# Kernel tuning notes

Hardware: AMD Instinct MI355X
Metric: run time of the kernel (lower is better)

Reference implementation:

```python
import jax, jax.numpy as jnp
import numpy as np

N, E, H, G, L = 100000, 200000, 32, 100, 4
NODE_IN, EDGE_IN, NGRAPH = 6, 4, 50
EPS = 1e-5

def setup_inputs() -> dict:
    key = jax.random.key(0)
    ks = jax.random.split(key, 32)
    s = 0.05
    inp = {
        "x": jax.random.normal(ks[0], (N, NODE_IN), jnp.float32),
        "edge_index": jax.random.randint(ks[1], (2, E), 0, N, jnp.int64),
        "edge_attr": jax.random.normal(ks[2], (E, EDGE_IN), jnp.float32),
        "batch": jnp.sort(jax.random.randint(ks[3], (N,), 0, NGRAPH, jnp.int64)),
        # node embedding: Linear + ReLU + BatchNorm1d
        "w_embed": jax.random.normal(ks[4], (NODE_IN, H), jnp.float32) * s,
        "b_embed": jnp.zeros((H,), jnp.float32),
        "bn_gamma": jnp.ones((H,), jnp.float32),
        "bn_beta": jnp.zeros((H,), jnp.float32),
        # NNConv layers (stacked over L): edge MLP Linear(EDGE_IN,2H)->ReLU->Linear(2H,H*H), root weight, bias
        "conv_w1": jax.random.normal(ks[5], (L, EDGE_IN, 2 * H), jnp.float32) * s,
        "conv_b1": jnp.zeros((L, 2 * H), jnp.float32),
        "conv_w2": jax.random.normal(ks[6], (L, 2 * H, H * H), jnp.float32) * s,
        "conv_b2": jnp.zeros((L, H * H), jnp.float32),
        "conv_root": jax.random.normal(ks[7], (L, H, H), jnp.float32) * s,
        "conv_bias": jnp.zeros((L, H), jnp.float32),
        # heads
        "wk_w1": jax.random.normal(ks[8], (H, H), jnp.float32) * s,
        "wk_b1": jnp.zeros((H,), jnp.float32),
        "wk_w2": jax.random.normal(ks[9], (H, 1), jnp.float32) * s,
        "wk_b2": jnp.zeros((1,), jnp.float32),
        "uj_w1": jax.random.normal(ks[10], (H, H), jnp.float32) * s,
        "uj_b1": jnp.zeros((H,), jnp.float32),
        "uj_w2": jax.random.normal(ks[11], (H, G), jnp.float32) * s,
        "uj_b2": jnp.zeros((G,), jnp.float32),
        "zk_w1": jax.random.normal(ks[12], (H, H), jnp.float32) * s,
        "zk_b1": jnp.zeros((H,), jnp.float32),
        "zk_w2": jax.random.normal(ks[13], (H, G), jnp.float32) * s,
        "zk_b2": jnp.zeros((G,), jnp.float32),
    }
    return inp

def _mlp2(h, w1, b1, w2, b2):
    return jax.nn.relu(h @ w1 + b1) @ w2 + b2

def _forward(x, edge_index, edge_attr, batch,
             w_embed, b_embed, bn_gamma, bn_beta,
             conv_w1, conv_b1, conv_w2, conv_b2, conv_root, conv_bias,
             wk_w1, wk_b1, wk_w2, wk_b2,
             uj_w1, uj_b1, uj_w2, uj_b2,
             zk_w1, zk_b1, zk_w2, zk_b2):
    src, dst = edge_index[0], edge_index[1]
    # node embed: Linear -> ReLU -> BatchNorm1d (training-mode batch stats)
    h = jax.nn.relu(x @ w_embed + b_embed)
    mu = h.mean(axis=0)
    var = ((h - mu) ** 2).mean(axis=0)  # biased, as torch BN uses for normalization
    h = (h - mu) * jax.lax.rsqrt(var + EPS) * bn_gamma + bn_beta
    # in-degree for mean aggregation
    deg = jax.ops.segment_sum(jnp.ones((E,), h.dtype), dst, num_segments=N)
    inv_deg = (1.0 / jnp.maximum(deg, 1.0))[:, None]
    for l in range(L):
        # per-edge weight matrix from edge MLP: [E, H, H]
        W = _mlp2(edge_attr, conv_w1[l], conv_b1[l], conv_w2[l], conv_b2[l]).reshape(E, H, H)
        msg = jnp.einsum('ei,eio->eo', h[src], W)  # gather + per-edge matmul
        agg = jax.ops.segment_sum(msg, dst, num_segments=N) * inv_deg  # scatter-mean
        h = jax.nn.relu(agg + h @ conv_root[l] + conv_bias[l])
    # global mean pool over graphs
    cnt = jax.ops.segment_sum(jnp.ones((N,), h.dtype), batch, num_segments=NGRAPH)
    hg = jax.ops.segment_sum(h, batch, num_segments=NGRAPH) / jnp.maximum(cnt, 1.0)[:, None]
    wk = _mlp2(hg, wk_w1, wk_b1, wk_w2, wk_b2).squeeze(-1)
    uj = _mlp2(hg, uj_w1, uj_b1, uj_w2, uj_b2)
    zk = _mlp2(hg, zk_w1, zk_b1, zk_w2, zk_b2)
    return wk, uj, zk

def reference(x, edge_index, edge_attr, batch,
              w_embed, b_embed, bn_gamma, bn_beta,
              conv_w1, conv_b1, conv_w2, conv_b2, conv_root, conv_bias,
              wk_w1, wk_b1, wk_w2, wk_b2,
              uj_w1, uj_b1, uj_w2, uj_b2,
              zk_w1, zk_b1, zk_w2, zk_b2):
    return _forward(x, edge_index, edge_attr, batch,
                    w_embed, b_embed, bn_gamma, bn_beta,
                    conv_w1, conv_b1, conv_w2, conv_b2, conv_root, conv_bias,
                    wk_w1, wk_b1, wk_w2, wk_b2,
                    uj_w1, uj_b1, uj_w2, uj_b2,
                    zk_w1, zk_b1, zk_w2, zk_b2)
```

## Files before the change

### kernel.cpp

```cpp
#include <hip/hip_runtime.h>

#define NN 100000
#define NE 200000
#define HH 32
#define NL 4
#define NGR 50
#define GOUT 100
#define NODE_IN 6
#define NEB 782

typedef __attribute__((ext_vector_type(8))) short bf16x8;
typedef __attribute__((ext_vector_type(4))) float f32x4;

__device__ __forceinline__ unsigned short bf16_rne(float x) {
    unsigned int b = __float_as_uint(x);
    b += 0x7FFFu + ((b >> 16) & 1u);
    return (unsigned short)(b >> 16);
}
__device__ __forceinline__ float bf16_f(unsigned short h) {
    return __uint_as_float(((unsigned int)h) << 16);
}

__global__ __launch_bounds__(256) void split_w2(const float* __restrict__ w2,
                                                unsigned short* __restrict__ w2h,
                                                unsigned short* __restrict__ w2l)
{
    int id = blockIdx.x * 256 + threadIdx.x;
    if (id >= NL * 64 * 1024) return;
    int l = id >> 16, rem = id & 65535;
    int k = rem >> 10, n = rem & 1023;
    float v = w2[id];
    unsigned short hi = bf16_rne(v);
    float lov = v - bf16_f(hi);
    unsigned short lo = bf16_rne(lov);
    int out = l * 65536 + n * 64 + k;
    w2h[out] = hi;
    w2l[out] = lo;
}

__global__ __launch_bounds__(256) void embed_kernel(
    const float* __restrict__ x, const float* __restrict__ w,
    const float* __restrict__ b, float* __restrict__ h0)
{
    int nid = blockIdx.x * 256 + threadIdx.x;
    if (nid >= NN) return;
    float xv[NODE_IN];
    #pragma unroll
    for (int d = 0; d < NODE_IN; ++d) xv[d] = x[nid * NODE_IN + d];
    float4* op = (float4*)(h0 + (size_t)nid * HH);
    #pragma unroll
    for (int q = 0; q < 8; ++q) {
        float4 r;
        float* rp = (float*)&r;
        #pragma unroll
        for (int u = 0; u < 4; ++u) {
            int j = q * 4 + u;
            float a = b[j];
            #pragma unroll
            for (int d = 0; d < NODE_IN; ++d) a = fmaf(xv[d], w[d * HH + j], a);
            rp[u] = fmaxf(a, 0.f);
        }
        op[q] = r;
    }
}

__global__ __launch_bounds__(256) void stats_kernel(const float* __restrict__ h0,
                                                    float* __restrict__ stats)
{
    __shared__ float ls[64];
    int tid = threadIdx.x;
    if (tid < 64) ls[tid] = 0.f;
    __syncthreads();
    float s[4] = {0.f, 0.f, 0.f, 0.f};
    float q[4] = {0.f, 0.f, 0.f, 0.f};
    const float4* h4 = (const float4*)h0;
    const int total = NN * HH / 4;
    for (int idx = blockIdx.x * 256 + tid; idx < total; idx += 128 * 256) {
        float4 v = h4[idx];
        s[0] += v.x; q[0] += v.x * v.x;
        s[1] += v.y; q[1] += v.y * v.y;
        s[2] += v.z; q[2] += v.z * v.z;
        s[3] += v.w; q[3] += v.w * v.w;
    }
    int c0 = (tid * 4) & 31;
    #pragma unroll
    for (int u = 0; u < 4; ++u) {
        atomicAdd(&ls[c0 + u], s[u]);
        atomicAdd(&ls[32 + c0 + u], q[u]);
    }
    __syncthreads();
    if (tid < 64) unsafeAtomicAdd(&stats[tid], ls[tid]);
}

__global__ __launch_bounds__(256) void deg_kernel(const int* __restrict__ ei,
                                                  float* __restrict__ deg)
{
    int e = blockIdx.x * 256 + threadIdx.x;
    if (e >= NE) return;
    unsafeAtomicAdd(&deg[ei[NE + e]], 1.0f);
}

__global__ void bn_finalize(const float* __restrict__ stats,
                            const float* __restrict__ gamma,
                            const float* __restrict__ beta,
                            float* __restrict__ bnp)
{
    int j = threadIdx.x;
    if (j >= HH) return;
    const float invn = 1.0f / (float)NN;
    float mu  = stats[j] * invn;
    float var = stats[32 + j] * invn - mu * mu;
    float rs  = 1.0f / sqrtf(var + 1e-5f);
    float sc  = rs * gamma[j];
    bnp[j]      = sc;
    bnp[32 + j] = beta[j] - mu * sc;
}

__global__ __launch_bounds__(256) void bn_apply(float* __restrict__ h,
                                                const float* __restrict__ bnp)
{
    int idx = blockIdx.x * 256 + threadIdx.x;
    if (idx >= NN * HH / 4) return;
    float4 v = ((float4*)h)[idx];
    int j = (idx * 4) & 31;
    v.x = fmaf(v.x, bnp[j + 0], bnp[32 + j + 0]);
    v.y = fmaf(v.y, bnp[j + 1], bnp[32 + j + 1]);
    v.z = fmaf(v.z, bnp[j + 2], bnp[32 + j + 2]);
    v.w = fmaf(v.w, bnp[j + 3], bnp[32 + j + 3]);
    ((float4*)h)[idx] = v;
}

__global__ __launch_bounds__(256) void edge_mfma(
    const float* __restrict__ h, const int* __restrict__ ei,
    const float* __restrict__ ea,
    const float* __restrict__ w1, const float* __restrict__ b1,
    const unsigned short* __restrict__ w2h, const unsigned short* __restrict__ w2l,
    const float* __restrict__ b2, float* __restrict__ agg)
{
    __shared__ float hT[32 * 256];
    __shared__ float b2l[1024];
    __shared__ int   dstl[256];
    __shared__ unsigned short Bh[2][4096];
    __shared__ unsigned short Bl[2][4096];

    const int tid  = threadIdx.x;
    const int w    = tid >> 6;
    const int lane = tid & 63;
    const int l15  = lane & 15;
    const int lg   = lane >> 4;
    const int eb   = blockIdx.x * 256;

    const unsigned int* gh = (const unsigned int*)w2h;
    const unsigned int* gl = (const unsigned int*)w2l;
    const int wavebase = tid & ~63;

    auto stage = [&](int c2, int buf) {
        #pragma unroll
        for (int q = 0; q < 2; ++q) {
            int g = q * 256 + tid;
            int n = g >> 3, j = g & 7;
            int gi = ((c2 * 64 + n) << 3) + (j ^ (n & 7));
            int lb = (q * 256 + wavebase) * 8;
            __builtin_amdgcn_global_load_lds(
                (const __attribute__((address_space(1))) unsigned int*)(gh + (size_t)gi * 4),
                (__attribute__((address_space(3))) unsigned int*)(&Bh[buf][0] + lb), 16, 0, 0);
            __builtin_amdgcn_global_load_lds(
                (const __attribute__((address_space(1))) unsigned int*)(gl + (size_t)gi * 4),
                (__attribute__((address_space(3))) unsigned int*)(&Bl[buf][0] + lb), 16, 0, 0);
        }
    };

    stage(0, 0);

    {
        int e = eb + tid;
        int s = 0, d = 0;
        if (e < NE) { s = ei[e]; d = ei[NE + e]; }
        dstl[tid] = d;
        const float4* hp = (const float4*)(h + (size_t)s * HH);
        #pragma unroll
        for (int q = 0; q < 8; ++q) {
            float4 v = hp[q];
            hT[(q * 4 + 0) * 256 + tid] = v.x;
            hT[(q * 4 + 1) * 256 + tid] = v.y;
            hT[(q * 4 + 2) * 256 + tid] = v.z;
            hT[(q * 4 + 3) * 256 + tid] = v.w;
        }
        ((float4*)b2l)[tid] = ((const float4*)b2)[tid];
    }

    bf16x8 thi[4][2], tlo[4][2];
    #pragma unroll
    for (int et = 0; et < 4; ++et) {
        int e = eb + w * 64 + et * 16 + l15;
        bool ev = (e < NE);
        float4 eav = make_float4(0.f, 0.f, 0.f, 0.f);
        if (ev) eav = *(const float4*)(ea + (size_t)e * 4);
        #pragma unroll
        for (int ks = 0; ks < 2; ++ks) {
            int k0 = ks * 32 + lg * 8;
            #pragma unroll
            for (int j = 0; j < 8; ++j) {
                float t = b1[k0 + j];
                t = fmaf(eav.x, w1[0 * 64 + k0 + j], t);
                t = fmaf(eav.y, w1[1 * 64 + k0 + j], t);
                t = fmaf(eav.z, w1[2 * 64 + k0 + j], t);
                t = fmaf(eav.w, w1[3 * 64 + k0 + j], t);
                t = ev ? fmaxf(t, 0.f) : 0.f;
                unsigned short hi = bf16_rne(t);
                float lov = t - bf16_f(hi);
                unsigned short lo = bf16_rne(lov);
                thi[et][ks][j] = (short)hi;
                tlo[et][ks][j] = (short)lo;
            }
        }
    }

    float acc0[4][4], acc1[4][4];
    #pragma unroll
    for (int et = 0; et < 4; ++et)
        #pragma unroll
        for (int r = 0; r < 4; ++r) { acc0[et][r] = 0.f; acc1[et][r] = 0.f; }

    for (int c2 = 0; c2 < 16; ++c2) {
        const int buf = c2 & 1;
        __syncthreads();
        if (c2 < 15) stage(c2 + 1, buf ^ 1);

        #pragma unroll
        for (int ntp = 0; ntp < 2; ++ntp) {
            const int i = c2 * 2 + ntp;
            float4 h4[4];
            #pragma unroll
            for (int et = 0; et < 4; ++et)
                h4[et] = *(const float4*)&hT[i * 256 + wavebase + et * 16 + lg * 4];
            #pragma unroll
            for (int half = 0; half < 2; ++half) {
                int nt = ntp * 2 + half;
                int nl = nt * 16 + l15;
                int swz = (nl & 7) << 4;
                const char* bhrow = (const char*)&Bh[buf][0] + nl * 128;
                const char* blrow = (const char*)&Bl[buf][0] + nl * 128;
                bf16x8 Bh0 = *(const bf16x8*)(bhrow + (( 0 + lg * 16) ^ swz));
                bf16x8 Bl0 = *(const bf16x8*)(blrow + (( 0 + lg * 16) ^ swz));
                bf16x8 Bh1 = *(const bf16x8*)(bhrow + ((64 + lg * 16) ^ swz));
                bf16x8 Bl1 = *(const bf16x8*)(blrow + ((64 + lg * 16) ^ swz));
                float b2v = b2l[c2 * 64 + nt * 16 + l15];
                #pragma unroll
                for (int et = 0; et < 4; ++et) {
                    f32x4 G = {0.f, 0.f, 0.f, 0.f};
                    G = __builtin_amdgcn_mfma_f32_16x16x32_bf16(thi[et][0], Bh0, G, 0, 0, 0);
                    G = __builtin_amdgcn_mfma_f32_16x16x32_bf16(tlo[et][0], Bh0, G, 0, 0, 0);
                    G = __builtin_amdgcn_mfma_f32_16x16x32_bf16(thi[et][0], Bl0, G, 0, 0, 0);
                    G = __builtin_amdgcn_mfma_f32_16x16x32_bf16(thi[et][1], Bh1, G, 0, 0, 0);
                    G = __builtin_amdgcn_mfma_f32_16x16x32_bf16(tlo[et][1], Bh1, G, 0, 0, 0);
                    G = __builtin_amdgcn_mfma_f32_16x16x32_bf16(thi[et][1], Bl1, G, 0, 0, 0);
                    if (half == 0) {
                        acc0[et][0] = fmaf(h4[et].x, G[0] + b2v, acc0[et][0]);
                        acc0[et][1] = fmaf(h4[et].y, G[1] + b2v, acc0[et][1]);
                        acc0[et][2] = fmaf(h4[et].z, G[2] + b2v, acc0[et][2]);
                        acc0[et][3] = fmaf(h4[et].w, G[3] + b2v, acc0[et][3]);
                    } else {
                        acc1[et][0] = fmaf(h4[et].x, G[0] + b2v, acc1[et][0]);
                        acc1[et][1] = fmaf(h4[et].y, G[1] + b2v, acc1[et][1]);
                        acc1[et][2] = fmaf(h4[et].z, G[2] + b2v, acc1[et][2]);
                        acc1[et][3] = fmaf(h4[et].w, G[3] + b2v, acc1[et][3]);
                    }
                }
            }
        }
    }

    #pragma unroll
    for (int et = 0; et < 4; ++et) {
        int eloc = wavebase + et * 16 + lg * 4;
        int4 d4 = *(const int4*)&dstl[eloc];
        #pragma unroll
        for (int r = 0; r < 4; ++r) {
            int eg = eb + eloc + r;
            if (eg < NE) {
                int dd = (r == 0) ? d4.x : (r == 1) ? d4.y : (r == 2) ? d4.z : d4.w;
                unsafeAtomicAdd(agg + (size_t)dd * HH + l15,      acc0[et][r]);
                unsafeAtomicAdd(agg + (size_t)dd * HH + 16 + l15, acc1[et][r]);
            }
        }
    }
}

__global__ __launch_bounds__(256) void node_kernel(
    const float* __restrict__ h, const float* __restrict__ agg,
    const float* __restrict__ deg, const float* __restrict__ root,
    const float* __restrict__ bias, float* __restrict__ hout)
{
    int nid = blockIdx.x * 256 + threadIdx.x;
    if (nid >= NN) return;
    float hv[HH];
    {
        const float4* hp = (const float4*)(h + nid * HH);
        #pragma unroll
        for (int q = 0; q < 8; ++q) {
            float4 v = hp[q];
            hv[4*q+0] = v.x; hv[4*q+1] = v.y; hv[4*q+2] = v.z; hv[4*q+3] = v.w;
        }
    }
    float inv = 1.0f / fmaxf(deg[nid], 1.0f);
    float acc[HH];
    #pragma unroll
    for (int o = 0; o < HH; ++o) acc[o] = bias[o];
    #pragma unroll
    for (int i = 0; i < HH; ++i) {
        float hi = hv[i];
        #pragma unroll
        for (int o = 0; o < HH; ++o) acc[o] = fmaf(hi, root[i * HH + o], acc[o]);
    }
    const float4* av = (const float4*)(agg + nid * HH);
    #pragma unroll
    for (int q = 0; q < 8; ++q) {
        float4 a = av[q];
        float4 r;
        r.x = fmaxf(fmaf(a.x, inv, acc[4*q+0]), 0.f);
        r.y = fmaxf(fmaf(a.y, inv, acc[4*q+1]), 0.f);
        r.z = fmaxf(fmaf(a.z, inv, acc[4*q+2]), 0.f);
        r.w = fmaxf(fmaf(a.w, inv, acc[4*q+3]), 0.f);
        ((float4*)(hout + nid * HH))[q] = r;
    }
}

__global__ __launch_bounds__(256) void pool_kernel(
    const float* __restrict__ h, const int* __restrict__ batch,
    float* __restrict__ pool, float* __restrict__ cnt)
{
    __shared__ float lp[NGR * HH];
    __shared__ float lc[NGR];
    int tid = threadIdx.x;
    for (int i = tid; i < NGR * HH; i += 256) lp[i] = 0.f;
    for (int i = tid; i < NGR; i += 256) lc[i] = 0.f;
    __syncthreads();
    int nid = blockIdx.x * 256 + tid;
    if (nid < NN) {
        int g = batch[nid];
        atomicAdd(&lc[g], 1.0f);
        #pragma unroll
        for (int j = 0; j < HH; ++j) atomicAdd(&lp[g * HH + j], h[nid * HH + j]);
    }
    __syncthreads();
    for (int i = tid; i < NGR * HH; i += 256)
        if (lp[i] != 0.f) unsafeAtomicAdd(&pool[i], lp[i]);
    for (int i = tid; i < NGR; i += 256)
        if (lc[i] != 0.f) unsafeAtomicAdd(&cnt[i], lc[i]);
}

__global__ __launch_bounds__(256) void heads_kernel(
    const float* __restrict__ pool, const float* __restrict__ cnt,
    const float* __restrict__ wkw1, const float* __restrict__ wkb1,
    const float* __restrict__ wkw2, const float* __restrict__ wkb2,
    const float* __restrict__ ujw1, const float* __restrict__ ujb1,
    const float* __restrict__ ujw2, const float* __restrict__ ujb2,
    const float* __restrict__ zkw1, const float* __restrict__ zkb1,
    const float* __restrict__ zkw2, const float* __restrict__ zkb2,
    float* __restrict__ out)
{
    __shared__ float hg[NGR * HH];
    __shared__ float hid[NGR * HH];
    int tid = threadIdx.x;
    int head = blockIdx.x;
    const float *w1, *b1, *w2, *b2;
    if (head == 0)      { w1 = wkw1; b1 = wkb1; w2 = wkw2; b2 = wkb2; }
    else if (head == 1) { w1 = ujw1; b1 = ujb1; w2 = ujw2; b2 = ujb2; }
    else                { w1 = zkw1; b1 = zkb1; w2 = zkw2; b2 = zkb2; }
    for (int i = tid; i < NGR * HH; i += 256) {
        int g = i >> 5;
        hg[i] = pool[i] / fmaxf(cnt[g], 1.0f);
    }
    __syncthreads();
    for (int i = tid; i < NGR * HH; i += 256) {
        int g = i >> 5, c = i & 31;
        float a = b1[c];
        for (int j = 0; j < HH; ++j) a = fmaf(hg[g * HH + j], w1[j * HH + c], a);
        hid[i] = fmaxf(a, 0.f);
    }
    __syncthreads();
    if (head == 0) {
        if (tid < NGR) {
            float a = b2[0];
            for (int c = 0; c < HH; ++c) a = fmaf(hid[tid * HH + c], w2[c], a);
            out[tid] = a;
        }
    } else {
        float* ob = out + NGR + (head - 1) * NGR * GOUT;
        for (int i = tid; i < NGR * GOUT; i += 256) {
            int g = i / GOUT, u = i % GOUT;
            float a = b2[u];
            for (int c = 0; c < HH; ++c) a = fmaf(hid[g * HH + c], w2[c * GOUT + u], a);
            ob[i] = a;
        }
    }
}

extern "C" void kernel_launch(void* const* d_in, const int* in_sizes, int n_in,
                              void* d_out, int out_size, void* d_ws, size_t ws_size,
                              hipStream_t stream)
{
    const float* x     = (const float*)d_in[0];
    const int*   ei    = (const int*)d_in[1];
    const float* ea    = (const float*)d_in[2];
    const int*   batch = (const int*)d_in[3];
    const float* w_emb = (const float*)d_in[4];
    const float* b_emb = (const float*)d_in[5];
    const float* gamma = (const float*)d_in[6];
    const float* beta  = (const float*)d_in[7];
    const float* cw1   = (const float*)d_in[8];
    const float* cb1   = (const float*)d_in[9];
    const float* cw2   = (const float*)d_in[10];
    const float* cb2   = (const float*)d_in[11];
    const float* croot = (const float*)d_in[12];
    const float* cbias = (const float*)d_in[13];
    float* out = (float*)d_out;

    unsigned short* w2h = (unsigned short*)d_ws;
    unsigned short* w2l = w2h + (size_t)NL * 65536;
    float* h0    = (float*)(w2l + (size_t)NL * 65536);
    float* h1    = h0 + (size_t)NN * HH;
    float* agg   = h1 + (size_t)NN * HH;
    float* deg   = agg + (size_t)NN * HH;
    float* stats = deg + NN;
    float* pool  = stats + 64;
    float* cnt   = pool + NGR * HH;
    float* bnp   = cnt + NGR;

    hipMemsetAsync(deg, 0, (size_t)(NN + 64 + NGR * HH + NGR) * sizeof(float), stream);

    split_w2<<<(NL * 65536) / 256, 256, 0, stream>>>(cw2, w2h, w2l);
    embed_kernel<<<(NN + 255) / 256, 256, 0, stream>>>(x, w_emb, b_emb, h0);
    stats_kernel<<<128, 256, 0, stream>>>(h0, stats);
    deg_kernel<<<(NE + 255) / 256, 256, 0, stream>>>(ei, deg);
    bn_finalize<<<1, 32, 0, stream>>>(stats, gamma, beta, bnp);
    bn_apply<<<(NN * HH / 4 + 255) / 256, 256, 0, stream>>>(h0, bnp);

    float* hc = h0;
    float* hn = h1;
    for (int l = 0; l < NL; ++l) {
        hipMemsetAsync(agg, 0, (size_t)NN * HH * sizeof(float), stream);
        edge_mfma<<<NEB, 256, 0, stream>>>(
            hc, ei, ea,
            cw1 + (size_t)l * 4 * 64, cb1 + (size_t)l * 64,
            w2h + (size_t)l * 65536, w2l + (size_t)l * 65536,
            cb2 + (size_t)l * 1024, agg);
        node_kernel<<<(NN + 255) / 256, 256, 0, stream>>>(
            hc, agg, deg, croot + (size_t)l * HH * HH, cbias + (size_t)l * HH, hn);
        float* t = hc; hc = hn; hn = t;
    }

    pool_kernel<<<(NN + 255) / 256, 256, 0, stream>>>(hc, batch, pool, cnt);
    heads_kernel<<<3, 256, 0, stream>>>(pool, cnt,
        (const float*)d_in[14], (const float*)d_in[15], (const float*)d_in[16], (const float*)d_in[17],
        (const float*)d_in[18], (const float*)d_in[19], (const float*)d_in[20], (const float*)d_in[21],
        (const float*)d_in[22], (const float*)d_in[23], (const float*)d_in[24], (const float*)d_in[25],
        out);
}
```

Baseline: 701.4 us.

## Replace atomic scatter-mean with CSR sort by destination and gather in node kernel

Builds a CSR structure with an integer degree count, a three-pass prefix scan and an atomic scatter of edge ids into a permutation sorted by destination. The edge kernel now processes edges in permuted order and writes per-edge messages to a dense buffer instead of issuing float atomics into agg. The node kernel sums each node's contiguous messages. This removes the per-layer memset and atomic contention, at the cost of an extra 25.6MB message buffer write and read per layer plus indirect loads through perm. It also drops the W2 double buffering in favour of a single buffer with an extra barrier and occupancy hint 3, and rewrites pooling to accumulate runs of the sorted batch before issuing atomics.

```diff
diff --git a/kernel.cpp b/kernel.cpp
--- a/kernel.cpp
+++ b/kernel.cpp
@@ -92,12 +92,12 @@
     if (tid < 64) unsafeAtomicAdd(&stats[tid], ls[tid]);
 }
 
-__global__ __launch_bounds__(256) void deg_kernel(const int* __restrict__ ei,
-                                                  float* __restrict__ deg)
+__global__ __launch_bounds__(256) void degi_kernel(const int* __restrict__ ei,
+                                                   int* __restrict__ degi)
 {
     int e = blockIdx.x * 256 + threadIdx.x;
     if (e >= NE) return;
-    unsafeAtomicAdd(&deg[ei[NE + e]], 1.0f);
+    atomicAdd(&degi[ei[NE + e]], 1);
 }
 
 __global__ void bn_finalize(const float* __restrict__ stats,
@@ -130,18 +130,79 @@
     ((float4*)h)[idx] = v;
 }
 
-__global__ __launch_bounds__(256) void edge_mfma(
+__global__ __launch_bounds__(256) void scan1(const int* __restrict__ degi,
+                                             int* __restrict__ rowptr,
+                                             int* __restrict__ bsum)
+{
+    __shared__ int sd[256];
+    int tid = threadIdx.x;
+    int i = blockIdx.x * 256 + tid;
+    int v = (i < NN) ? degi[i] : 0;
+    sd[tid] = v;
+    __syncthreads();
+    #pragma unroll
+    for (int off = 1; off < 256; off <<= 1) {
+        int t = (tid >= off) ? sd[tid - off] : 0;
+        __syncthreads();
+        sd[tid] += t;
+        __syncthreads();
+    }
+    if (i < NN) rowptr[i] = sd[tid] - v;
+    if (tid == 255) bsum[blockIdx.x] = sd[255];
+}
+
+__global__ __launch_bounds__(512) void scan2(int* __restrict__ bsum)
+{
+    __shared__ int sd[512];
+    int tid = threadIdx.x;
+    int v = (tid < 391) ? bsum[tid] : 0;
+    sd[tid] = v;
+    __syncthreads();
+    #pragma unroll
+    for (int off = 1; off < 512; off <<= 1) {
+        int t = (tid >= off) ? sd[tid - off] : 0;
+        __syncthreads();
+        sd[tid] += t;
+        __syncthreads();
+    }
+    if (tid < 391) bsum[tid] = sd[tid] - v;
+}
+
+__global__ __launch_bounds__(256) void scan3(int* __restrict__ rowptr,
+                                             const int* __restrict__ bsum,
+                                             int* __restrict__ cursor)
+{
+    int i = blockIdx.x * 256 + threadIdx.x;
+    if (i < NN) {
+        int r = rowptr[i] + bsum[blockIdx.x];
+        rowptr[i] = r;
+        cursor[i] = r;
+    }
+    if (i == 0) rowptr[NN] = NE;
+}
+
+__global__ __launch_bounds__(256) void scatter_k(const int* __restrict__ ei,
+                                                 int* __restrict__ cursor,
+                                                 int* __restrict__ perm)
+{
+    int e = blockIdx.x * 256 + threadIdx.x;
+    if (e >= NE) return;
+    int d = ei[NE + e];
+    int pos = atomicAdd(&cursor[d], 1);
+    perm[pos] = e;
+}
+
+__global__ __launch_bounds__(256, 3) void edge_mfma(
     const float* __restrict__ h, const int* __restrict__ ei,
-    const float* __restrict__ ea,
+    const float* __restrict__ ea, const int* __restrict__ perm,
     const float* __restrict__ w1, const float* __restrict__ b1,
     const unsigned short* __restrict__ w2h, const unsigned short* __restrict__ w2l,
-    const float* __restrict__ b2, float* __restrict__ agg)
+    const float* __restrict__ b2, float* __restrict__ msg)
 {
     __shared__ float hT[32 * 256];
     __shared__ float b2l[1024];
-    __shared__ int   dstl[256];
-    __shared__ unsigned short Bh[2][4096];
-    __shared__ unsigned short Bl[2][4096];
+    __shared__ unsigned short Bh[4096];
+    __shared__ unsigned short Bl[4096];
 
     const int tid  = threadIdx.x;
     const int w    = tid >> 6;
@@ -149,12 +210,12 @@
     const int l15  = lane & 15;
     const int lg   = lane >> 4;
     const int eb   = blockIdx.x * 256;
+    const int wavebase = tid & ~63;
 
     const unsigned int* gh = (const unsigned int*)w2h;
     const unsigned int* gl = (const unsigned int*)w2l;
-    const int wavebase = tid & ~63;
-
-    auto stage = [&](int c2, int buf) {
+
+    auto stage = [&](int c2) {
         #pragma unroll
         for (int q = 0; q < 2; ++q) {
             int g = q * 256 + tid;
@@ -163,20 +224,17 @@
             int lb = (q * 256 + wavebase) * 8;
             __builtin_amdgcn_global_load_lds(
                 (const __attribute__((address_space(1))) unsigned int*)(gh + (size_t)gi * 4),
-                (__attribute__((address_space(3))) unsigned int*)(&Bh[buf][0] + lb), 16, 0, 0);
+                (__attribute__((address_space(3))) unsigned int*)(&Bh[0] + lb), 16, 0, 0);
             __builtin_amdgcn_global_load_lds(
                 (const __attribute__((address_space(1))) unsigned int*)(gl + (size_t)gi * 4),
-                (__attribute__((address_space(3))) unsigned int*)(&Bl[buf][0] + lb), 16, 0, 0);
+                (__attribute__((address_space(3))) unsigned int*)(&Bl[0] + lb), 16, 0, 0);
         }
     };
-
-    stage(0, 0);
 
     {
         int e = eb + tid;
-        int s = 0, d = 0;
-        if (e < NE) { s = ei[e]; d = ei[NE + e]; }
-        dstl[tid] = d;
+        int pe = (e < NE) ? perm[e] : 0;
+        int s  = (e < NE) ? ei[pe] : 0;
         const float4* hp = (const float4*)(h + (size_t)s * HH);
         #pragma unroll
         for (int q = 0; q < 8; ++q) {
@@ -192,10 +250,11 @@
     bf16x8 thi[4][2], tlo[4][2];
     #pragma unroll
     for (int et = 0; et < 4; ++et) {
-        int e = eb + w * 64 + et * 16 + l15;
-        bool ev = (e < NE);
+        int e2 = eb + wavebase + et * 16 + l15;
+        bool ev = (e2 < NE);
+        int pe2 = ev ? perm[e2] : 0;
         float4 eav = make_float4(0.f, 0.f, 0.f, 0.f);
-        if (ev) eav = *(const float4*)(ea + (size_t)e * 4);
+        if (ev) eav = *(const float4*)(ea + (size_t)pe2 * 4);
         #pragma unroll
         for (int ks = 0; ks < 2; ++ks) {
             int k0 = ks * 32 + lg * 8;
@@ -223,9 +282,9 @@
         for (int r = 0; r < 4; ++r) { acc0[et][r] = 0.f; acc1[et][r] = 0.f; }
 
     for (int c2 = 0; c2 < 16; ++c2) {
-        const int buf = c2 & 1;
         __syncthreads();
-        if (c2 < 15) stage(c2 + 1, buf ^ 1);
+        stage(c2);
+        __syncthreads();
 
         #pragma unroll
         for (int ntp = 0; ntp < 2; ++ntp) {
@@ -239,8 +298,8 @@
                 int nt = ntp * 2 + half;
                 int nl = nt * 16 + l15;
                 int swz = (nl & 7) << 4;
-                const char* bhrow = (const char*)&Bh[buf][0] + nl * 128;
-                const char* blrow = (const char*)&Bl[buf][0] + nl * 128;
+                const char* bhrow = (const char*)&Bh[0] + nl * 128;
+                const char* blrow = (const char*)&Bl[0] + nl * 128;
                 bf16x8 Bh0 = *(const bf16x8*)(bhrow + (( 0 + lg * 16) ^ swz));
                 bf16x8 Bl0 = *(const bf16x8*)(blrow + (( 0 + lg * 16) ^ swz));
                 bf16x8 Bh1 = *(const bf16x8*)(bhrow + ((64 + lg * 16) ^ swz));
@@ -273,37 +332,34 @@
 
     #pragma unroll
     for (int et = 0; et < 4; ++et) {
-        int eloc = wavebase + et * 16 + lg * 4;
-        int4 d4 = *(const int4*)&dstl[eloc];
         #pragma unroll
         for (int r = 0; r < 4; ++r) {
-            int eg = eb + eloc + r;
-            if (eg < NE) {
-                int dd = (r == 0) ? d4.x : (r == 1) ? d4.y : (r == 2) ? d4.z : d4.w;
-                unsafeAtomicAdd(agg + (size_t)dd * HH + l15,      acc0[et][r]);
-                unsafeAtomicAdd(agg + (size_t)dd * HH + 16 + l15, acc1[et][r]);
+            int row = eb + wavebase + et * 16 + lg * 4 + r;
+            if (row < NE) {
+                msg[(size_t)row * HH + l15]      = acc0[et][r];
+                msg[(size_t)row * HH + 16 + l15] = acc1[et][r];
             }
         }
     }
 }
 
 __global__ __launch_bounds__(256) void node_kernel(
-    const float* __restrict__ h, const float* __restrict__ agg,
-    const float* __restrict__ deg, const float* __restrict__ root,
+    const float* __restrict__ h, const float* __restrict__ msg,
+    const int* __restrict__ rowptr, const float* __restrict__ root,
     const float* __restrict__ bias, float* __restrict__ hout)
 {
     int nid = blockIdx.x * 256 + threadIdx.x;
     if (nid >= NN) return;
+    int j0 = rowptr[nid], j1 = rowptr[nid + 1];
     float hv[HH];
     {
-        const float4* hp = (const float4*)(h + nid * HH);
+        const float4* hp = (const float4*)(h + (size_t)nid * HH);
         #pragma unroll
         for (int q = 0; q < 8; ++q) {
             float4 v = hp[q];
             hv[4*q+0] = v.x; hv[4*q+1] = v.y; hv[4*q+2] = v.z; hv[4*q+3] = v.w;
         }
     }
-    float inv = 1.0f / fmaxf(deg[nid], 1.0f);
     float acc[HH];
     #pragma unroll
     for (int o = 0; o < HH; ++o) acc[o] = bias[o];
@@ -313,16 +369,27 @@
         #pragma unroll
         for (int o = 0; o < HH; ++o) acc[o] = fmaf(hi, root[i * HH + o], acc[o]);
     }
-    const float4* av = (const float4*)(agg + nid * HH);
+    float s[HH];
+    #pragma unroll
+    for (int o = 0; o < HH; ++o) s[o] = 0.f;
+    for (int j = j0; j < j1; ++j) {
+        const float4* mp = (const float4*)(msg + (size_t)j * HH);
+        #pragma unroll
+        for (int q = 0; q < 8; ++q) {
+            float4 m = mp[q];
+            s[4*q+0] += m.x; s[4*q+1] += m.y; s[4*q+2] += m.z; s[4*q+3] += m.w;
+        }
+    }
+    float inv = 1.0f / fmaxf((float)(j1 - j0), 1.0f);
+    float4* op = (float4*)(hout + (size_t)nid * HH);
     #pragma unroll
     for (int q = 0; q < 8; ++q) {
-        float4 a = av[q];
         float4 r;
-        r.x = fmaxf(fmaf(a.x, inv, acc[4*q+0]), 0.f);
-        r.y = fmaxf(fmaf(a.y, inv, acc[4*q+1]), 0.f);
-        r.z = fmaxf(fmaf(a.z, inv, acc[4*q+2]), 0.f);
-        r.w = fmaxf(fmaf(a.w, inv, acc[4*q+3]), 0.f);
-        ((float4*)(hout + nid * HH))[q] = r;
+        r.x = fmaxf(fmaf(s[4*q+0], inv, acc[4*q+0]), 0.f);
+        r.y = fmaxf(fmaf(s[4*q+1], inv, acc[4*q+1]), 0.f);
+        r.z = fmaxf(fmaf(s[4*q+2], inv, acc[4*q+2]), 0.f);
+        r.w = fmaxf(fmaf(s[4*q+3], inv, acc[4*q+3]), 0.f);
+        op[q] = r;
     }
 }
 
@@ -334,20 +401,34 @@
     __shared__ float lc[NGR];
     int tid = threadIdx.x;
     for (int i = tid; i < NGR * HH; i += 256) lp[i] = 0.f;
-    for (int i = tid; i < NGR; i += 256) lc[i] = 0.f;
-    __syncthreads();
-    int nid = blockIdx.x * 256 + tid;
-    if (nid < NN) {
-        int g = batch[nid];
-        atomicAdd(&lc[g], 1.0f);
-        #pragma unroll
-        for (int j = 0; j < HH; ++j) atomicAdd(&lp[g * HH + j], h[nid * HH + j]);
+    if (tid < NGR) lc[tid] = 0.f;
+    __syncthreads();
+    int c = tid & 31, grp = tid >> 5;
+    int base = blockIdx.x * 1024 + grp * 128;
+    int curg = -1;
+    float acc = 0.f, cn = 0.f;
+    for (int s = 0; s < 128; ++s) {
+        int n = base + s;
+        if (n >= NN) break;
+        int g = batch[n];
+        if (g != curg) {
+            if (curg >= 0) {
+                atomicAdd(&lp[curg * HH + c], acc);
+                if (c == 0) atomicAdd(&lc[curg], cn);
+            }
+            curg = g; acc = 0.f; cn = 0.f;
+        }
+        acc += h[(size_t)n * HH + c];
+        cn += 1.f;
+    }
+    if (curg >= 0) {
+        atomicAdd(&lp[curg * HH + c], acc);
+        if (c == 0) atomicAdd(&lc[curg], cn);
     }
     __syncthreads();
     for (int i = tid; i < NGR * HH; i += 256)
         if (lp[i] != 0.f) unsafeAtomicAdd(&pool[i], lp[i]);
-    for (int i = tid; i < NGR; i += 256)
-        if (lc[i] != 0.f) unsafeAtomicAdd(&cnt[i], lc[i]);
+    if (tid < NGR && lc[tid] != 0.f) unsafeAtomicAdd(&cnt[tid], lc[tid]);
 }
 
 __global__ __launch_bounds__(256) void heads_kernel(
@@ -418,40 +499,48 @@
     float* out = (float*)d_out;
 
     unsigned short* w2h = (unsigned short*)d_ws;
-    unsigned short* w2l = w2h + (size_t)NL * 65536;
-    float* h0    = (float*)(w2l + (size_t)NL * 65536);
-    float* h1    = h0 + (size_t)NN * HH;
-    float* agg   = h1 + (size_t)NN * HH;
-    float* deg   = agg + (size_t)NN * HH;
-    float* stats = deg + NN;
-    float* pool  = stats + 64;
-    float* cnt   = pool + NGR * HH;
-    float* bnp   = cnt + NGR;
-
-    hipMemsetAsync(deg, 0, (size_t)(NN + 64 + NGR * HH + NGR) * sizeof(float), stream);
+    unsigned short* w2l = w2h + 262144;
+    float* msg    = (float*)(w2l + 262144);
+    float* h0     = msg + (size_t)NE * HH;
+    float* h1     = h0 + (size_t)NN * HH;
+    int*   rowptr = (int*)(h1 + (size_t)NN * HH);
+    int*   cursor = rowptr + 100004;
+    int*   perm   = cursor + NN;
+    int*   degi   = perm + NE;
+    int*   bsum   = degi + NN;
+    float* stats  = (float*)(bsum + 512);
+    float* pool   = stats + 64;
+    float* cnt    = pool + NGR * HH;
+    float* bnp    = cnt + NGR;
+
+    hipMemsetAsync(degi, 0, (size_t)(NN + 512 + 64 + NGR * HH + NGR) * sizeof(int), stream);
 
     split_w2<<<(NL * 65536) / 256, 256, 0, stream>>>(cw2, w2h, w2l);
     embed_kernel<<<(NN + 255) / 256, 256, 0, stream>>>(x, w_emb, b_emb, h0);
     stats_kernel<<<128, 256, 0, stream>>>(h0, stats);
-    deg_kernel<<<(NE + 255) / 256, 256, 0, stream>>>(ei, deg);
+    degi_kernel<<<NEB, 256, 0, stream>>>(ei, degi);
     bn_finalize<<<1, 32, 0, stream>>>(stats, gamma, beta, bnp);
     bn_apply<<<(NN * HH / 4 + 255) / 256, 256, 0, stream>>>(h0, bnp);
+
+    scan1<<<391, 256, 0, stream>>>(degi, rowptr, bsum);
+    scan2<<<1, 512, 0, stream>>>(bsum);
+    scan3<<<391, 256, 0, stream>>>(rowptr, bsum, cursor);
+    scatter_k<<<NEB, 256, 0, stream>>>(ei, cursor, perm);
 
     float* hc = h0;
     float* hn = h1;
     for (int l = 0; l < NL; ++l) {
-        hipMemsetAsync(agg, 0, (size_t)NN * HH * sizeof(float), stream);
         edge_mfma<<<NEB, 256, 0, stream>>>(
-            hc, ei, ea,
+            hc, ei, ea, perm,
             cw1 + (size_t)l * 4 * 64, cb1 + (size_t)l * 64,
             w2h + (size_t)l * 65536, w2l + (size_t)l * 65536,
-            cb2 + (size_t)l * 1024, agg);
+            cb2 + (size_t)l * 1024, msg);
         node_kernel<<<(NN + 255) / 256, 256, 0, stream>>>(
-            hc, agg, deg, croot + (size_t)l * HH * HH, cbias + (size_t)l * HH, hn);
+            hc, msg, rowptr, croot + (size_t)l * HH * HH, cbias + (size_t)l * HH, hn);
         float* t = hc; hc = hn; hn = t;
     }
 
-    pool_kernel<<<(NN + 255) / 256, 256, 0, stream>>>(hc, batch, pool, cnt);
+    pool_kernel<<<(NN + 1023) / 1024, 256, 0, stream>>>(hc, batch, pool, cnt);
     heads_kernel<<<3, 256, 0, stream>>>(pool, cnt,
         (const float*)d_in[14], (const float*)d_in[15], (const float*)d_in[16], (const float*)d_in[17],
         (const float*)d_in[18], (const float*)d_in[19], (const float*)d_in[20], (const float*)d_in[21],
```

Result: slower. 972.7 us (+38.7%).
